# Kernel tuning notes

Measured on AMD Instinct MI355X. Metric: run time of the kernel, lower is better.

## Reference

```python
import jax, jax.numpy as jnp
import numpy as np

B = 16384
QD = 2048   # query_dim
KD = 1024   # key_dim
HID = 1024  # hidden_dim = min(QD, KD)
NH = 16     # num_heads
HD = HID // NH  # head_dim = 64
LN_EPS = 1e-5


def _ln(x, w, b):
    m = jnp.mean(x, axis=-1, keepdims=True)
    v = jnp.mean((x - m) ** 2, axis=-1, keepdims=True)
    return (x - m) * jax.lax.rsqrt(v + LN_EPS) * w + b


def _lin(x, W, b):
    return x @ W.T + b


def setup_inputs() -> dict:
    key = jax.random.key(0)
    ks = jax.random.split(key, 12)
    p = lambda k, shape: jax.random.normal(k, shape, jnp.float32) * 0.02
    return dict(
        query_features=jax.random.normal(ks[0], (B, QD), jnp.float32),
        key_features=jax.random.normal(ks[1], (B, KD), jnp.float32),
        Wq=p(ks[2], (HID, QD)), bq=jnp.zeros((HID,), jnp.float32),
        ln_q_w=jnp.ones((HID,), jnp.float32), ln_q_b=jnp.zeros((HID,), jnp.float32),
        Wk=p(ks[3], (HID, KD)), bk=jnp.zeros((HID,), jnp.float32),
        ln_k_w=jnp.ones((HID,), jnp.float32), ln_k_b=jnp.zeros((HID,), jnp.float32),
        Wvq=p(ks[4], (HID, QD)), bvq=jnp.zeros((HID,), jnp.float32),
        Wvk=p(ks[5], (HID, KD)), bvk=jnp.zeros((HID,), jnp.float32),
        Wo=p(ks[6], (QD, HID)), bo=jnp.zeros((QD,), jnp.float32),
        ln_o_w=jnp.ones((QD,), jnp.float32), ln_o_b=jnp.zeros((QD,), jnp.float32),
        Wg1=p(ks[7], (HID, QD + KD)), bg1=jnp.zeros((HID,), jnp.float32),
        Wg2=p(ks[8], (1, HID)), bg2=jnp.zeros((1,), jnp.float32),
        Wc1=p(ks[9], (HID, QD + KD)), bc1=jnp.zeros((HID,), jnp.float32),
        Wc2=p(ks[10], (1, HID)), bc2=jnp.zeros((1,), jnp.float32),
    )


def reference(query_features, key_features,
              Wq, bq, ln_q_w, ln_q_b,
              Wk, bk, ln_k_w, ln_k_b,
              Wvq, bvq, Wvk, bvk,
              Wo, bo, ln_o_w, ln_o_b,
              Wg1, bg1, Wg2, bg2,
              Wc1, bc1, Wc2, bc2):
    b = query_features.shape[0]
    q = _ln(_lin(query_features, Wq, bq), ln_q_w, ln_q_b)      # [B, HID]
    k = _ln(_lin(key_features, Wk, bk), ln_k_w, ln_k_b)        # [B, HID]
    v_q = _lin(query_features, Wvq, bvq)  # computed in torch but unused
    v_k = _lin(key_features, Wvk, bvk)    # [B, HID]
    q = q.reshape(b, NH, HD)
    k = k.reshape(b, NH, HD)
    v_k = v_k.reshape(b, NH, HD)
    # NOTE: attention mixes over the HEAD axis (j == num_heads), per original einsum
    scores = jnp.einsum('bhd,bjd->bhj', q, k) / np.sqrt(HD).astype(np.float32)
    attn = jax.nn.softmax(scores, axis=-1)  # dropout p effectively 0 / eval mode
    attended = jnp.einsum('bhj,bjd->bhd', attn, v_k).reshape(b, HID)
    output = _ln(_lin(attended, Wo, bo), ln_o_w, ln_o_b)       # [B, QD]
    combined = jnp.concatenate([query_features, key_features], axis=1)  # [B, QD+KD]
    gate = jax.nn.sigmoid(_lin(jax.nn.gelu(_lin(combined, Wg1, bg1), approximate=False), Wg2, bg2))
    chem = jax.nn.sigmoid(_lin(jax.nn.gelu(_lin(combined, Wc1, bc1), approximate=False), Wc2, bc2))
    effective_gate = gate * chem  # [B, 1]
    return query_features + effective_gate * output
```

## Files before the change

### kernel.cpp

```cpp
#include <hip/hip_runtime.h>
#include <stdint.h>

#define QD 2048
#define KD 1024
#define HID 1024
#define NH 16
#define HD 64
#define CMBD 3072

typedef float  f32x4   __attribute__((ext_vector_type(4)));
typedef short  short8  __attribute__((ext_vector_type(8)));
typedef short  short4v __attribute__((ext_vector_type(4)));
typedef float  float4v __attribute__((ext_vector_type(4)));

__device__ inline float bf2f(short s) {
  unsigned u = ((unsigned)(unsigned short)s) << 16;
  return __builtin_bit_cast(float, u);
}
__device__ inline short f2bf(float f) {
  unsigned u = __builtin_bit_cast(unsigned, f);
  u = u + 0x7fff + ((u >> 16) & 1);
  return (short)(u >> 16);
}

__global__ void cvt_bf16(const float* __restrict__ s, short* __restrict__ d) {
  size_t i = ((size_t)blockIdx.x * blockDim.x + threadIdx.x) * 4;
  float4v v = *(const float4v*)(s + i);
  short4v o;
  o[0] = f2bf(v[0]); o[1] = f2bf(v[1]); o[2] = f2bf(v[2]); o[3] = f2bf(v[3]);
  *(short4v*)(d + i) = o;
}

__global__ void cvt_concat(const float* __restrict__ s, short* __restrict__ d,
                           int ncols4, int ldd) {
  int i = blockIdx.x * blockDim.x + threadIdx.x;
  int row = i / ncols4;
  int c4  = i - row * ncols4;
  float4v v = *(const float4v*)(s + (size_t)row * (ncols4 * 4) + c4 * 4);
  short4v o;
  o[0] = f2bf(v[0]); o[1] = f2bf(v[1]); o[2] = f2bf(v[2]); o[3] = f2bf(v[3]);
  *(short4v*)(d + (size_t)row * ldd + c4 * 4) = o;
}

#define EPI_NONE 0
#define EPI_GELU 1

typedef const __attribute__((address_space(1))) void gvoid_t;
typedef __attribute__((address_space(3))) void lvoid_t;

#define WAIT_VM(n)  asm volatile("s_waitcnt vmcnt(" #n ")" ::: "memory")
#define WAIT_LGKM0  asm volatile("s_waitcnt lgkmcnt(0)" ::: "memory")

template<int EPI>
__global__ __launch_bounds__(512, 2)
void gemm256(const short* __restrict__ A, size_t lda,
             const short* __restrict__ W,
             const float* __restrict__ bias,
             short* __restrict__ C, int N, int K) {
  extern __shared__ short ls[];
  const int tid  = threadIdx.x;
  const int lane = tid & 63;
  const int wave = tid >> 6;
  const int wm = wave >> 2, wn = wave & 3;
  const int fr = lane & 15, kq4 = lane >> 4;

  const int nwg = gridDim.x * gridDim.y;
  const int lin = blockIdx.y * gridDim.x + blockIdx.x;
  const int cpx = nwg >> 3;
  const int nid = (lin & 7) * cpx + (lin >> 3);
  const int bx = nid % gridDim.x, by = nid / gridDim.x;
  const size_t rowBase = (size_t)by * 256;
  const size_t colBase = (size_t)bx * 256;

  const int NT = K >> 5;

  f32x4 acc[8][4];
#pragma unroll
  for (int mi = 0; mi < 8; mi++)
#pragma unroll
    for (int ni = 0; ni < 4; ni++) acc[mi][ni] = (f32x4){0.f, 0.f, 0.f, 0.f};

  const int frsw = (kq4 ^ ((fr >> 1) & 3)) * 8;
  const int aoff = (wm * 128 + fr) * 32 + frsw;
  const int boff = 8192 + (wn * 64 + fr) * 32 + frsw;

  const int grow  = tid >> 2;
  const int slotx = (tid & 3) ^ ((tid >> 3) & 3);
  const short* pA0 = A + (rowBase + grow) * lda + slotx * 8;
  const short* pA1 = pA0 + (size_t)128 * lda;
  const short* pB0 = W + (colBase + grow) * (size_t)K + slotx * 8;
  const short* pB1 = pB0 + (size_t)128 * K;
  short* const dst0 = ls + tid * 8;

  auto STAGE = [&](int slot) {
    short* d = dst0 + slot * 16384;
    __builtin_amdgcn_global_load_lds((gvoid_t*)pA0, (lvoid_t*)d,            16, 0, 0);
    __builtin_amdgcn_global_load_lds((gvoid_t*)pA1, (lvoid_t*)(d + 4096),   16, 0, 0);
    __builtin_amdgcn_global_load_lds((gvoid_t*)pB0, (lvoid_t*)(d + 8192),   16, 0, 0);
    __builtin_amdgcn_global_load_lds((gvoid_t*)pB1, (lvoid_t*)(d + 12288),  16, 0, 0);
    pA0 += 32; pA1 += 32; pB0 += 32; pB1 += 32;
  };

  STAGE(0); STAGE(1); STAGE(2);
  WAIT_VM(8);
  __builtin_amdgcn_s_barrier();

  for (int t = 0; t < NT; ++t) {
    const short* sl = ls + (t & 3) * 16384;
    if (t + 3 < NT) STAGE((t + 3) & 3);

    short8 af[8], bf[4];
#pragma unroll
    for (int m = 0; m < 8; m++) af[m] = *(const short8*)(sl + aoff + m * 512);
#pragma unroll
    for (int n = 0; n < 4; n++) bf[n] = *(const short8*)(sl + boff + n * 512);

    __builtin_amdgcn_s_setprio(1);
#pragma unroll
    for (int m = 0; m < 8; m++)
#pragma unroll
      for (int n = 0; n < 4; n++)
        acc[m][n] = __builtin_amdgcn_mfma_f32_16x16x32_bf16(af[m], bf[n], acc[m][n], 0, 0, 0);
    __builtin_amdgcn_s_setprio(0);

    WAIT_LGKM0;
    const int rem = NT - 2 - t;
    if (rem >= 2)      { WAIT_VM(8); }
    else if (rem == 1) { WAIT_VM(4); }
    else               { WAIT_VM(0); }
    __builtin_amdgcn_s_barrier();
  }

#pragma unroll
  for (int mi = 0; mi < 8; mi++) {
    const size_t row0 = rowBase + wm * 128 + mi * 16 + kq4 * 4;
#pragma unroll
    for (int ni = 0; ni < 4; ni++) {
      const int col = (int)colBase + wn * 64 + ni * 16 + fr;
      const float bv = bias[col];
#pragma unroll
      for (int j = 0; j < 4; j++) {
        float x = acc[mi][ni][j] + bv;
        if (EPI == EPI_GELU) x = 0.5f * x * (1.f + erff(x * 0.70710678118f));
        C[(row0 + j) * (size_t)N + col] = f2bf(x);
      }
    }
  }
}

__device__ inline float2 block_sum2(float a, float b, float* sc) {
#pragma unroll
  for (int o = 32; o >= 1; o >>= 1) {
    a += __shfl_down(a, o);
    b += __shfl_down(b, o);
  }
  const int lane = threadIdx.x & 63, w = threadIdx.x >> 6;
  const int nw = blockDim.x >> 6;
  if (lane == 0) { sc[w * 2] = a; sc[w * 2 + 1] = b; }
  __syncthreads();
  float ra = 0.f, rb = 0.f;
  for (int i = 0; i < nw; i++) { ra += sc[i * 2]; rb += sc[i * 2 + 1]; }
  __syncthreads();
  return make_float2(ra, rb);
}

__global__ __launch_bounds__(256)
void attn_ln(const short* __restrict__ qp, const short* __restrict__ kv,
             const float* __restrict__ lnqw, const float* __restrict__ lnqb,
             const float* __restrict__ lnkw, const float* __restrict__ lnkb,
             short* __restrict__ att) {
  __shared__ float qs[HID];
  __shared__ float ks[NH * 65];
  __shared__ float vs[HID];
  __shared__ float aw[256];
  __shared__ float red[8];
  const int t = threadIdx.x;
  const size_t row = blockIdx.x;

  short4v q4 = *(const short4v*)(qp + row * HID + t * 4);
  short4v k4 = *(const short4v*)(kv + row * 2048 + t * 4);
  short4v v4 = *(const short4v*)(kv + row * 2048 + 1024 + t * 4);
  float qv[4], kvv[4];
  float sq = 0.f, sqq = 0.f, sk = 0.f, skk = 0.f;
#pragma unroll
  for (int i = 0; i < 4; i++) {
    qv[i] = bf2f(q4[i]); sq += qv[i]; sqq += qv[i] * qv[i];
    kvv[i] = bf2f(k4[i]); sk += kvv[i]; skk += kvv[i] * kvv[i];
  }
  float2 rq = block_sum2(sq, sqq, red);
  float mq = rq.x / HID, vq = rq.y / HID - mq * mq;
  float rsq = rsqrtf(vq + 1e-5f);
  float2 rk = block_sum2(sk, skk, red);
  float mk = rk.x / HID, vv = rk.y / HID - mk * mk;
  float rsk = rsqrtf(vv + 1e-5f);
#pragma unroll
  for (int i = 0; i < 4; i++) {
    const int idx = t * 4 + i;
    qs[idx] = (qv[i] - mq) * rsq * lnqw[idx] + lnqb[idx];
    ks[(idx >> 6) * 65 + (idx & 63)] = (kvv[i] - mk) * rsk * lnkw[idx] + lnkb[idx];
    vs[idx] = bf2f(v4[i]);
  }
  __syncthreads();

  const int h = t >> 4, j = t & 15;
  float s = 0.f;
#pragma unroll 8
  for (int d = 0; d < 64; d++) s += qs[h * 64 + d] * ks[j * 65 + d];
  s *= 0.125f;
  float mx = s;
#pragma unroll
  for (int o = 8; o >= 1; o >>= 1) mx = fmaxf(mx, __shfl_xor(mx, o, 16));
  float e = __expf(s - mx);
  float sum = e;
#pragma unroll
  for (int o = 8; o >= 1; o >>= 1) sum += __shfl_xor(sum, o, 16);
  aw[t] = e / sum;
  __syncthreads();

  const int dB = (t & 15) * 4;
  float o0 = 0.f, o1 = 0.f, o2 = 0.f, o3 = 0.f;
#pragma unroll
  for (int jj = 0; jj < 16; jj++) {
    const float w = aw[h * 16 + jj];
    const float* vp = &vs[jj * 64 + dB];
    o0 += w * vp[0]; o1 += w * vp[1]; o2 += w * vp[2]; o3 += w * vp[3];
  }
  short4v o4;
  o4[0] = f2bf(o0); o4[1] = f2bf(o1); o4[2] = f2bf(o2); o4[3] = f2bf(o3);
  *(short4v*)(att + row * HID + h * 64 + dB) = o4;
}

__global__ __launch_bounds__(256)
void gate_kernel(const short* __restrict__ hgc,
                 const float* __restrict__ wg2, const float* __restrict__ bg2,
                 const float* __restrict__ wc2, const float* __restrict__ bc2,
                 float* __restrict__ eg) {
  __shared__ float red[8];
  const int t = threadIdx.x;
  const size_t row = blockIdx.x;
  short4v g4 = *(const short4v*)(hgc + row * 2048 + t * 4);
  short4v c4 = *(const short4v*)(hgc + row * 2048 + 1024 + t * 4);
  float sg = 0.f, sc = 0.f;
#pragma unroll
  for (int i = 0; i < 4; i++) {
    sg += bf2f(g4[i]) * wg2[t * 4 + i];
    sc += bf2f(c4[i]) * wc2[t * 4 + i];
  }
  float2 r = block_sum2(sg, sc, red);
  if (t == 0) {
    float g = 1.f / (1.f + __expf(-(r.x + bg2[0])));
    float c = 1.f / (1.f + __expf(-(r.y + bc2[0])));
    eg[row] = g * c;
  }
}

__global__ __launch_bounds__(256)
void final_kernel(const short* __restrict__ opre, const float* __restrict__ qf,
                  const float* __restrict__ eg,
                  const float* __restrict__ lnow, const float* __restrict__ lnob,
                  float* __restrict__ out) {
  __shared__ float red[8];
  const int t = threadIdx.x;
  const size_t row = blockIdx.x;
  short8 o8 = *(const short8*)(opre + row * QD + t * 8);
  float x[8];
  float s = 0.f, ss = 0.f;
#pragma unroll
  for (int i = 0; i < 8; i++) { x[i] = bf2f(o8[i]); s += x[i]; ss += x[i] * x[i]; }
  float2 r = block_sum2(s, ss, red);
  float m = r.x / QD, v = r.y / QD - m * m;
  float rs = rsqrtf(v + 1e-5f);
  float g = eg[row];
  float4v oa, ob;
#pragma unroll
  for (int i = 0; i < 8; i++) {
    const int c = t * 8 + i;
    float y = (x[i] - m) * rs * lnow[c] + lnob[c];
    float r2 = qf[row * QD + c] + g * y;
    if (i < 4) oa[i] = r2; else ob[i - 4] = r2;
  }
  *(float4v*)(out + row * QD + t * 8) = oa;
  *(float4v*)(out + row * QD + t * 8 + 4) = ob;
}

extern "C" void kernel_launch(void* const* d_in, const int* in_sizes, int n_in,
                              void* d_out, int out_size, void* d_ws, size_t ws_size,
                              hipStream_t stream) {
  const float* qf   = (const float*)d_in[0];
  const float* kf   = (const float*)d_in[1];
  const float* Wq   = (const float*)d_in[2];
  const float* bq   = (const float*)d_in[3];
  const float* lnqw = (const float*)d_in[4];
  const float* lnqb = (const float*)d_in[5];
  const float* Wk   = (const float*)d_in[6];
  const float* bk   = (const float*)d_in[7];
  const float* lnkw = (const float*)d_in[8];
  const float* lnkb = (const float*)d_in[9];
  const float* Wvk  = (const float*)d_in[12];
  const float* bvk  = (const float*)d_in[13];
  const float* Wo   = (const float*)d_in[14];
  const float* bo   = (const float*)d_in[15];
  const float* lnow = (const float*)d_in[16];
  const float* lnob = (const float*)d_in[17];
  const float* Wg1  = (const float*)d_in[18];
  const float* bg1  = (const float*)d_in[19];
  const float* Wg2  = (const float*)d_in[20];
  const float* bg2  = (const float*)d_in[21];
  const float* Wc1  = (const float*)d_in[22];
  const float* bc1  = (const float*)d_in[23];
  const float* Wc2  = (const float*)d_in[24];
  const float* bc2  = (const float*)d_in[25];

  const int rows = in_sizes[0] / QD;

  char* ws = (char*)d_ws;
  size_t off = 0;
  auto alloc = [&](size_t bytes) -> char* {
    char* p = ws + off;
    off += (bytes + 255) & ~(size_t)255;
    return p;
  };
  short* cmb  = (short*)alloc((size_t)rows * CMBD * 2);
  short* wqb  = (short*)alloc((size_t)HID * QD * 2);
  short* wkv  = (short*)alloc((size_t)2 * HID * KD * 2);
  short* wob  = (short*)alloc((size_t)QD * HID * 2);
  short* wgc  = (short*)alloc((size_t)2 * HID * CMBD * 2);
  short* hgc  = (short*)alloc((size_t)rows * 2048 * 2);
  short* qp   = (short*)alloc((size_t)rows * HID * 2);
  short* kvp  = (short*)alloc((size_t)rows * 2048 * 2);
  float* eg   = (float*)alloc((size_t)rows * 4);
  float* bgc  = (float*)alloc(2048 * 4);
  float* bkv  = (float*)alloc(2048 * 4);
  short* att  = hgc;
  short* opre = cmb;

  hipMemcpyAsync(bgc, bg1, HID * 4, hipMemcpyDeviceToDevice, stream);
  hipMemcpyAsync(bgc + HID, bc1, HID * 4, hipMemcpyDeviceToDevice, stream);
  hipMemcpyAsync(bkv, bk, HID * 4, hipMemcpyDeviceToDevice, stream);
  hipMemcpyAsync(bkv + HID, bvk, HID * 4, hipMemcpyDeviceToDevice, stream);

  cvt_concat<<<rows * 2, 256, 0, stream>>>(qf, cmb, QD / 4, CMBD);
  cvt_concat<<<rows, 256, 0, stream>>>(kf, cmb + QD, KD / 4, CMBD);
  cvt_bf16<<<(HID * QD / 4) / 256, 256, 0, stream>>>(Wq, wqb);
  cvt_bf16<<<(HID * KD / 4) / 256, 256, 0, stream>>>(Wk, wkv);
  cvt_bf16<<<(HID * KD / 4) / 256, 256, 0, stream>>>(Wvk, wkv + (size_t)HID * KD);
  cvt_bf16<<<(QD * HID / 4) / 256, 256, 0, stream>>>(Wo, wob);
  cvt_bf16<<<(HID * CMBD / 4) / 256, 256, 0, stream>>>(Wg1, wgc);
  cvt_bf16<<<(HID * CMBD / 4) / 256, 256, 0, stream>>>(Wc1, wgc + (size_t)HID * CMBD);

  hipFuncSetAttribute((const void*)gemm256<EPI_GELU>,
                      hipFuncAttributeMaxDynamicSharedMemorySize, 131072);
  hipFuncSetAttribute((const void*)gemm256<EPI_NONE>,
                      hipFuncAttributeMaxDynamicSharedMemorySize, 131072);

  const dim3 blk(512);
  const int mt = rows / 256;
  const size_t lds = 131072;

  gemm256<EPI_GELU><<<dim3(2048 / 256, mt), blk, lds, stream>>>(cmb, CMBD, wgc, bgc, hgc, 2048, CMBD);
  gate_kernel<<<rows, 256, 0, stream>>>(hgc, Wg2, bg2, Wc2, bc2, eg);
  gemm256<EPI_NONE><<<dim3(1024 / 256, mt), blk, lds, stream>>>(cmb, CMBD, wqb, bq, qp, 1024, QD);
  gemm256<EPI_NONE><<<dim3(2048 / 256, mt), blk, lds, stream>>>(cmb + QD, CMBD, wkv, bkv, kvp, 2048, KD);
  attn_ln<<<rows, 256, 0, stream>>>(qp, kvp, lnqw, lnqb, lnkw, lnkb, att);
  gemm256<EPI_NONE><<<dim3(2048 / 256, mt), blk, lds, stream>>>(att, HID, wob, bo, opre, 2048, HID);
  final_kernel<<<rows, 256, 0, stream>>>(opre, qf, eg, lnow, lnob, (float*)d_out);
}
```

Measured before the change: 656.0 us.

## Split GEMM main loop into two phases interleaving LDS reads, staging, and MFMA

The main loop of the bf16 GEMM is split into two half-tiles. Each half reads part of the A fragments from LDS, issues half of the next global-to-LDS prefetch (A then B), hits a barrier, and runs half of the MFMAs. The goal is to interleave memory issue with matrix math and spread the prefetch traffic through the loop instead of issuing it all at once. The explicit lgkmcnt wait is removed and an extra barrier is added per iteration, which relies on the compiler inserting the LDS waits and adds synchronisation cost.

```diff
diff --git a/kernel.cpp b/kernel.cpp
--- a/kernel.cpp
+++ b/kernel.cpp
@@ -49,7 +49,6 @@
 typedef __attribute__((address_space(3))) void lvoid_t;
 
 #define WAIT_VM(n)  asm volatile("s_waitcnt vmcnt(" #n ")" ::: "memory")
-#define WAIT_LGKM0  asm volatile("s_waitcnt lgkmcnt(0)" ::: "memory")
 
 template<int EPI>
 __global__ __launch_bounds__(512, 2)
@@ -92,38 +91,55 @@
   const short* pB1 = pB0 + (size_t)128 * K;
   short* const dst0 = ls + tid * 8;
 
-  auto STAGE = [&](int slot) {
+  auto STAGE_A = [&](int slot) {
     short* d = dst0 + slot * 16384;
-    __builtin_amdgcn_global_load_lds((gvoid_t*)pA0, (lvoid_t*)d,            16, 0, 0);
-    __builtin_amdgcn_global_load_lds((gvoid_t*)pA1, (lvoid_t*)(d + 4096),   16, 0, 0);
-    __builtin_amdgcn_global_load_lds((gvoid_t*)pB0, (lvoid_t*)(d + 8192),   16, 0, 0);
-    __builtin_amdgcn_global_load_lds((gvoid_t*)pB1, (lvoid_t*)(d + 12288),  16, 0, 0);
-    pA0 += 32; pA1 += 32; pB0 += 32; pB1 += 32;
+    __builtin_amdgcn_global_load_lds((gvoid_t*)pA0, (lvoid_t*)d,           16, 0, 0);
+    __builtin_amdgcn_global_load_lds((gvoid_t*)pA1, (lvoid_t*)(d + 4096),  16, 0, 0);
+    pA0 += 32; pA1 += 32;
   };
-
-  STAGE(0); STAGE(1); STAGE(2);
+  auto STAGE_B = [&](int slot) {
+    short* d = dst0 + slot * 16384;
+    __builtin_amdgcn_global_load_lds((gvoid_t*)pB0, (lvoid_t*)(d + 8192),  16, 0, 0);
+    __builtin_amdgcn_global_load_lds((gvoid_t*)pB1, (lvoid_t*)(d + 12288), 16, 0, 0);
+    pB0 += 32; pB1 += 32;
+  };
+
+  STAGE_A(0); STAGE_B(0); STAGE_A(1); STAGE_B(1); STAGE_A(2); STAGE_B(2);
   WAIT_VM(8);
   __builtin_amdgcn_s_barrier();
 
   for (int t = 0; t < NT; ++t) {
     const short* sl = ls + (t & 3) * 16384;
-    if (t + 3 < NT) STAGE((t + 3) & 3);
-
-    short8 af[8], bf[4];
-#pragma unroll
-    for (int m = 0; m < 8; m++) af[m] = *(const short8*)(sl + aoff + m * 512);
+    const bool dostage = (t + 3 < NT);
+    const int ssl = (t + 3) & 3;
+    short8 af[4], ag[4], bf[4];
+
+#pragma unroll
+    for (int m = 0; m < 4; m++) af[m] = *(const short8*)(sl + aoff + m * 512);
 #pragma unroll
     for (int n = 0; n < 4; n++) bf[n] = *(const short8*)(sl + boff + n * 512);
-
+    if (dostage) STAGE_A(ssl);
+    __builtin_amdgcn_s_barrier();
     __builtin_amdgcn_s_setprio(1);
 #pragma unroll
-    for (int m = 0; m < 8; m++)
+    for (int m = 0; m < 4; m++)
 #pragma unroll
       for (int n = 0; n < 4; n++)
         acc[m][n] = __builtin_amdgcn_mfma_f32_16x16x32_bf16(af[m], bf[n], acc[m][n], 0, 0, 0);
     __builtin_amdgcn_s_setprio(0);
 
-    WAIT_LGKM0;
+#pragma unroll
+    for (int m = 0; m < 4; m++) ag[m] = *(const short8*)(sl + aoff + (m + 4) * 512);
+    if (dostage) STAGE_B(ssl);
+    __builtin_amdgcn_s_barrier();
+    __builtin_amdgcn_s_setprio(1);
+#pragma unroll
+    for (int m = 0; m < 4; m++)
+#pragma unroll
+      for (int n = 0; n < 4; n++)
+        acc[m + 4][n] = __builtin_amdgcn_mfma_f32_16x16x32_bf16(ag[m], bf[n], acc[m + 4][n], 0, 0, 0);
+    __builtin_amdgcn_s_setprio(0);
+
     const int rem = NT - 2 - t;
     if (rem >= 2)      { WAIT_VM(8); }
     else if (rem == 1) { WAIT_VM(4); }
```

Result: no change. 655.2 us (-0.1%).

## Double-buffer LDS fragment registers to overlap LDS reads with MFMA in GEMM

Applied to the files above, without the earlier changes.

The GEMM main loop now prefetches the next k-tile's A/B fragments from LDS into a second register set while the MFMAs consume the current set. The loop is unrolled by two to ping-pong between the register sets, and the vmcnt waits are retuned so a stage is ready one iteration earlier. This is meant to hide LDS read latency behind matrix-core work. In exchange it uses more VGPRs (24 short8 fragment registers), which could cause spills under launch_bounds(512,2), and it assumes NT is even.

```diff
diff --git a/kernel.cpp b/kernel.cpp
--- a/kernel.cpp
+++ b/kernel.cpp
@@ -49,7 +49,6 @@
 typedef __attribute__((address_space(3))) void lvoid_t;
 
 #define WAIT_VM(n)  asm volatile("s_waitcnt vmcnt(" #n ")" ::: "memory")
-#define WAIT_LGKM0  asm volatile("s_waitcnt lgkmcnt(0)" ::: "memory")
 
 template<int EPI>
 __global__ __launch_bounds__(512, 2)
@@ -94,41 +93,63 @@
 
   auto STAGE = [&](int slot) {
     short* d = dst0 + slot * 16384;
-    __builtin_amdgcn_global_load_lds((gvoid_t*)pA0, (lvoid_t*)d,            16, 0, 0);
-    __builtin_amdgcn_global_load_lds((gvoid_t*)pA1, (lvoid_t*)(d + 4096),   16, 0, 0);
-    __builtin_amdgcn_global_load_lds((gvoid_t*)pB0, (lvoid_t*)(d + 8192),   16, 0, 0);
-    __builtin_amdgcn_global_load_lds((gvoid_t*)pB1, (lvoid_t*)(d + 12288),  16, 0, 0);
+    __builtin_amdgcn_global_load_lds((gvoid_t*)pA0, (lvoid_t*)d,           16, 0, 0);
+    __builtin_amdgcn_global_load_lds((gvoid_t*)pA1, (lvoid_t*)(d + 4096),  16, 0, 0);
+    __builtin_amdgcn_global_load_lds((gvoid_t*)pB0, (lvoid_t*)(d + 8192),  16, 0, 0);
+    __builtin_amdgcn_global_load_lds((gvoid_t*)pB1, (lvoid_t*)(d + 12288), 16, 0, 0);
     pA0 += 32; pA1 += 32; pB0 += 32; pB1 += 32;
   };
 
   STAGE(0); STAGE(1); STAGE(2);
-  WAIT_VM(8);
+  WAIT_VM(4);
   __builtin_amdgcn_s_barrier();
 
-  for (int t = 0; t < NT; ++t) {
-    const short* sl = ls + (t & 3) * 16384;
-    if (t + 3 < NT) STAGE((t + 3) & 3);
-
-    short8 af[8], bf[4];
-#pragma unroll
-    for (int m = 0; m < 8; m++) af[m] = *(const short8*)(sl + aoff + m * 512);
-#pragma unroll
-    for (int n = 0; n < 4; n++) bf[n] = *(const short8*)(sl + boff + n * 512);
-
-    __builtin_amdgcn_s_setprio(1);
-#pragma unroll
-    for (int m = 0; m < 8; m++)
-#pragma unroll
-      for (int n = 0; n < 4; n++)
-        acc[m][n] = __builtin_amdgcn_mfma_f32_16x16x32_bf16(af[m], bf[n], acc[m][n], 0, 0, 0);
-    __builtin_amdgcn_s_setprio(0);
-
-    WAIT_LGKM0;
-    const int rem = NT - 2 - t;
-    if (rem >= 2)      { WAIT_VM(8); }
-    else if (rem == 1) { WAIT_VM(4); }
-    else               { WAIT_VM(0); }
-    __builtin_amdgcn_s_barrier();
+  short8 cf[12], nf[12];
+  {
+    const short* sl = ls;
+#pragma unroll
+    for (int m = 0; m < 8; m++) cf[m] = *(const short8*)(sl + aoff + m * 512);
+#pragma unroll
+    for (int n = 0; n < 4; n++) cf[8 + n] = *(const short8*)(sl + boff + n * 512);
+  }
+
+  for (int i = 0; i < NT; i += 2) {
+    {
+      if (i + 3 < NT) STAGE((i + 3) & 3);
+      const short* sl = ls + ((i + 1) & 3) * 16384;
+#pragma unroll
+      for (int m = 0; m < 8; m++) nf[m] = *(const short8*)(sl + aoff + m * 512);
+#pragma unroll
+      for (int n = 0; n < 4; n++) nf[8 + n] = *(const short8*)(sl + boff + n * 512);
+      __builtin_amdgcn_s_setprio(1);
+#pragma unroll
+      for (int m = 0; m < 8; m++)
+#pragma unroll
+        for (int n = 0; n < 4; n++)
+          acc[m][n] = __builtin_amdgcn_mfma_f32_16x16x32_bf16(cf[m], cf[8 + n], acc[m][n], 0, 0, 0);
+      __builtin_amdgcn_s_setprio(0);
+      if (i + 3 < NT) { WAIT_VM(4); } else { WAIT_VM(0); }
+      __builtin_amdgcn_s_barrier();
+    }
+    {
+      if (i + 4 < NT) STAGE((i + 4) & 3);
+      if (i + 2 < NT) {
+        const short* sl = ls + ((i + 2) & 3) * 16384;
+#pragma unroll
+        for (int m = 0; m < 8; m++) cf[m] = *(const short8*)(sl + aoff + m * 512);
+#pragma unroll
+        for (int n = 0; n < 4; n++) cf[8 + n] = *(const short8*)(sl + boff + n * 512);
+      }
+      __builtin_amdgcn_s_setprio(1);
+#pragma unroll
+      for (int m = 0; m < 8; m++)
+#pragma unroll
+        for (int n = 0; n < 4; n++)
+          acc[m][n] = __builtin_amdgcn_mfma_f32_16x16x32_bf16(nf[m], nf[8 + n], acc[m][n], 0, 0, 0);
+      __builtin_amdgcn_s_setprio(0);
+      if (i + 4 < NT) { WAIT_VM(4); } else { WAIT_VM(0); }
+      __builtin_amdgcn_s_barrier();
+    }
   }
 
 #pragma unroll
```

Measured after the change: 651.8 us. About the same (-0.6%).

## Shrink GEMM tile to 128x256 with double-buffered static LDS

Applied to the files above, without the earlier changes.

Replaces the 256x256 GEMM tile with a 128x256 tile and cuts the 4-stage async LDS pipeline to a 2-stage double buffer held in static shared memory (48 KB instead of 128 KB). Occupancy hint goes from 2 to 4 blocks per CU and the grid doubles in M. The aim is more resident waves and lower register and LDS pressure to hide latency. In exchange each A/B byte is reused less, and the shallower prefetch plus two barriers per K step may expose global-load latency.

```diff
diff --git a/kernel.cpp b/kernel.cpp
--- a/kernel.cpp
+++ b/kernel.cpp
@@ -49,15 +49,16 @@
 typedef __attribute__((address_space(3))) void lvoid_t;
 
 #define WAIT_VM(n)  asm volatile("s_waitcnt vmcnt(" #n ")" ::: "memory")
-#define WAIT_LGKM0  asm volatile("s_waitcnt lgkmcnt(0)" ::: "memory")
+
+#define SLOT 12288
 
 template<int EPI>
-__global__ __launch_bounds__(512, 2)
-void gemm256(const short* __restrict__ A, size_t lda,
+__global__ __launch_bounds__(512, 4)
+void gemm128(const short* __restrict__ A, size_t lda,
              const short* __restrict__ W,
              const float* __restrict__ bias,
              short* __restrict__ C, int N, int K) {
-  extern __shared__ short ls[];
+  __shared__ short ls[2 * SLOT];
   const int tid  = threadIdx.x;
   const int lane = tid & 63;
   const int wave = tid >> 6;
@@ -69,71 +70,63 @@
   const int cpx = nwg >> 3;
   const int nid = (lin & 7) * cpx + (lin >> 3);
   const int bx = nid % gridDim.x, by = nid / gridDim.x;
-  const size_t rowBase = (size_t)by * 256;
+  const size_t rowBase = (size_t)by * 128;
   const size_t colBase = (size_t)bx * 256;
 
   const int NT = K >> 5;
 
-  f32x4 acc[8][4];
-#pragma unroll
-  for (int mi = 0; mi < 8; mi++)
+  f32x4 acc[4][4];
+#pragma unroll
+  for (int mi = 0; mi < 4; mi++)
 #pragma unroll
     for (int ni = 0; ni < 4; ni++) acc[mi][ni] = (f32x4){0.f, 0.f, 0.f, 0.f};
 
   const int frsw = (kq4 ^ ((fr >> 1) & 3)) * 8;
-  const int aoff = (wm * 128 + fr) * 32 + frsw;
-  const int boff = 8192 + (wn * 64 + fr) * 32 + frsw;
+  const int aoff = (wm * 64 + fr) * 32 + frsw;
+  const int boff = 4096 + (wn * 64 + fr) * 32 + frsw;
 
   const int grow  = tid >> 2;
   const int slotx = (tid & 3) ^ ((tid >> 3) & 3);
   const short* pA0 = A + (rowBase + grow) * lda + slotx * 8;
-  const short* pA1 = pA0 + (size_t)128 * lda;
   const short* pB0 = W + (colBase + grow) * (size_t)K + slotx * 8;
   const short* pB1 = pB0 + (size_t)128 * K;
   short* const dst0 = ls + tid * 8;
 
   auto STAGE = [&](int slot) {
-    short* d = dst0 + slot * 16384;
-    __builtin_amdgcn_global_load_lds((gvoid_t*)pA0, (lvoid_t*)d,            16, 0, 0);
-    __builtin_amdgcn_global_load_lds((gvoid_t*)pA1, (lvoid_t*)(d + 4096),   16, 0, 0);
-    __builtin_amdgcn_global_load_lds((gvoid_t*)pB0, (lvoid_t*)(d + 8192),   16, 0, 0);
-    __builtin_amdgcn_global_load_lds((gvoid_t*)pB1, (lvoid_t*)(d + 12288),  16, 0, 0);
-    pA0 += 32; pA1 += 32; pB0 += 32; pB1 += 32;
+    short* d = dst0 + slot * SLOT;
+    __builtin_amdgcn_global_load_lds((gvoid_t*)pA0, (lvoid_t*)d,           16, 0, 0);
+    __builtin_amdgcn_global_load_lds((gvoid_t*)pB0, (lvoid_t*)(d + 4096),  16, 0, 0);
+    __builtin_amdgcn_global_load_lds((gvoid_t*)pB1, (lvoid_t*)(d + 8192),  16, 0, 0);
+    pA0 += 32; pB0 += 32; pB1 += 32;
   };
 
-  STAGE(0); STAGE(1); STAGE(2);
-  WAIT_VM(8);
-  __builtin_amdgcn_s_barrier();
+  STAGE(0);
 
   for (int t = 0; t < NT; ++t) {
-    const short* sl = ls + (t & 3) * 16384;
-    if (t + 3 < NT) STAGE((t + 3) & 3);
-
-    short8 af[8], bf[4];
-#pragma unroll
-    for (int m = 0; m < 8; m++) af[m] = *(const short8*)(sl + aoff + m * 512);
+    const short* sl = ls + (t & 1) * SLOT;
+    if (t + 1 < NT) { STAGE((t + 1) & 1); WAIT_VM(3); }
+    else            { WAIT_VM(0); }
+    __builtin_amdgcn_s_barrier();
+
+    short8 af[4], bf[4];
+#pragma unroll
+    for (int m = 0; m < 4; m++) af[m] = *(const short8*)(sl + aoff + m * 512);
 #pragma unroll
     for (int n = 0; n < 4; n++) bf[n] = *(const short8*)(sl + boff + n * 512);
 
     __builtin_amdgcn_s_setprio(1);
 #pragma unroll
-    for (int m = 0; m < 8; m++)
+    for (int m = 0; m < 4; m++)
 #pragma unroll
       for (int n = 0; n < 4; n++)
         acc[m][n] = __builtin_amdgcn_mfma_f32_16x16x32_bf16(af[m], bf[n], acc[m][n], 0, 0, 0);
     __builtin_amdgcn_s_setprio(0);
-
-    WAIT_LGKM0;
-    const int rem = NT - 2 - t;
-    if (rem >= 2)      { WAIT_VM(8); }
-    else if (rem == 1) { WAIT_VM(4); }
-    else               { WAIT_VM(0); }
     __builtin_amdgcn_s_barrier();
   }
 
 #pragma unroll
-  for (int mi = 0; mi < 8; mi++) {
-    const size_t row0 = rowBase + wm * 128 + mi * 16 + kq4 * 4;
+  for (int mi = 0; mi < 4; mi++) {
+    const size_t row0 = rowBase + wm * 64 + mi * 16 + kq4 * 4;
 #pragma unroll
     for (int ni = 0; ni < 4; ni++) {
       const int col = (int)colBase + wn * 64 + ni * 16 + fr;
@@ -348,20 +341,14 @@
   cvt_bf16<<<(HID * CMBD / 4) / 256, 256, 0, stream>>>(Wg1, wgc);
   cvt_bf16<<<(HID * CMBD / 4) / 256, 256, 0, stream>>>(Wc1, wgc + (size_t)HID * CMBD);
 
-  hipFuncSetAttribute((const void*)gemm256<EPI_GELU>,
-                      hipFuncAttributeMaxDynamicSharedMemorySize, 131072);
-  hipFuncSetAttribute((const void*)gemm256<EPI_NONE>,
-                      hipFuncAttributeMaxDynamicSharedMemorySize, 131072);
-
   const dim3 blk(512);
-  const int mt = rows / 256;
-  const size_t lds = 131072;
-
-  gemm256<EPI_GELU><<<dim3(2048 / 256, mt), blk, lds, stream>>>(cmb, CMBD, wgc, bgc, hgc, 2048, CMBD);
+  const int mt = rows / 128;
+
+  gemm128<EPI_GELU><<<dim3(2048 / 256, mt), blk, 0, stream>>>(cmb, CMBD, wgc, bgc, hgc, 2048, CMBD);
   gate_kernel<<<rows, 256, 0, stream>>>(hgc, Wg2, bg2, Wc2, bc2, eg);
-  gemm256<EPI_NONE><<<dim3(1024 / 256, mt), blk, lds, stream>>>(cmb, CMBD, wqb, bq, qp, 1024, QD);
-  gemm256<EPI_NONE><<<dim3(2048 / 256, mt), blk, lds, stream>>>(cmb + QD, CMBD, wkv, bkv, kvp, 2048, KD);
+  gemm128<EPI_NONE><<<dim3(1024 / 256, mt), blk, 0, stream>>>(cmb, CMBD, wqb, bq, qp, 1024, QD);
+  gemm128<EPI_NONE><<<dim3(2048 / 256, mt), blk, 0, stream>>>(cmb + QD, CMBD, wkv, bkv, kvp, 2048, KD);
   attn_ln<<<rows, 256, 0, stream>>>(qp, kvp, lnqw, lnqb, lnkw, lnkb, att);
-  gemm256<EPI_NONE><<<dim3(2048 / 256, mt), blk, lds, stream>>>(att, HID, wob, bo, opre, 2048, HID);
+  gemm128<EPI_NONE><<<dim3(2048 / 256, mt), blk, 0, stream>>>(att, HID, wob, bo, opre, 2048, HID);
   final_kernel<<<rows, 256, 0, stream>>>(opre, qf, eg, lnow, lnob, (float*)d_out);
 }
```

New measurement: 674.7 us. 2.8% more time.
